# Optimization experiments

Hardware: AMD Instinct MI355X
Metric: run time of the kernel (lower is better)

## Reference

```python
import jax, jax.numpy as jnp
import numpy as np

N, E, D, R = 50000, 800000, 128, 16
NUM_OBJS, NUM_ATTRS, L = 179, 10, 5
OBJ_DIM, ATTR_DIM, HID, NANGLE = 96, 32, 512, 24


def setup_inputs() -> dict:
    key = jax.random.key(0)
    ks = jax.random.split(key, 20)
    z = jax.random.normal(ks[0], (N, D), dtype=jnp.float32)
    objs = jax.random.randint(ks[1], (N,), 0, NUM_OBJS + 1)
    s = jax.random.randint(ks[2], (E,), 0, N)
    o = jax.random.randint(ks[3], (E,), 0, N)
    p = jax.random.randint(ks[4], (E,), 0, R)
    triples = jnp.stack([s, p, o], axis=1)
    attributes = jax.random.randint(ks[5], (N,), 0, NUM_ATTRS)
    w = 0.05
    obj_emb = jax.random.normal(ks[6], (NUM_OBJS + 1, OBJ_DIM), dtype=jnp.float32)
    attr_emb = jax.random.normal(ks[7], (NUM_ATTRS, ATTR_DIM), dtype=jnp.float32)
    Wrel = jax.random.normal(ks[8], (L, R, D, D), dtype=jnp.float32) * w
    Wroot = jax.random.normal(ks[9], (L, D, D), dtype=jnp.float32) * w
    bconv = jnp.zeros((L, D), dtype=jnp.float32)
    box_W1 = jax.random.normal(ks[10], (2 * D + ATTR_DIM, HID), dtype=jnp.float32) * w
    box_b1 = jnp.zeros((HID,), dtype=jnp.float32)
    box_W2 = jax.random.normal(ks[11], (HID, 6), dtype=jnp.float32) * w
    box_b2 = jnp.zeros((6,), dtype=jnp.float32)
    ang_W1 = jax.random.normal(ks[12], (2 * D, HID), dtype=jnp.float32) * w
    ang_b1 = jnp.zeros((HID,), dtype=jnp.float32)
    ang_W2 = jax.random.normal(ks[13], (HID, NANGLE), dtype=jnp.float32) * w
    ang_b2 = jnp.zeros((NANGLE,), dtype=jnp.float32)
    return dict(z=z, objs=objs, triples=triples, attributes=attributes,
                obj_emb=obj_emb, attr_emb=attr_emb, Wrel=Wrel, Wroot=Wroot,
                bconv=bconv, box_W1=box_W1, box_b1=box_b1, box_W2=box_W2,
                box_b2=box_b2, ang_W1=ang_W1, ang_b1=ang_b1, ang_W2=ang_W2,
                ang_b2=ang_b2)


def _rgcn_layer(x, s, o, p, Wr, Wroot_l, b):
    # relation-typed transform of all nodes: [N, R, D]
    h_rel = jnp.einsum('nd,rdf->nrf', x, Wr)
    msgs = h_rel[s, p]                                   # [E, D] gather
    # mean aggregation per (target, relation), as in PyG RGCNConv
    seg = o * R + p
    cnt = jax.ops.segment_sum(jnp.ones((s.shape[0],), x.dtype), seg,
                              num_segments=x.shape[0] * R)
    deg = jnp.maximum(cnt[seg], 1.0)
    agg = jax.ops.segment_sum(msgs / deg[:, None], o, num_segments=x.shape[0])
    return x @ Wroot_l + agg + b


def reference(z, objs, triples, attributes, obj_emb, attr_emb, Wrel, Wroot,
              bconv, box_W1, box_b1, box_W2, box_b2, ang_W1, ang_b1,
              ang_W2, ang_b2):
    s, p, o = triples[:, 0], triples[:, 1], triples[:, 2]
    attr_vecs = attr_emb[attributes]                     # [N, 32]
    obj_vecs = jnp.concatenate([obj_emb[objs], attr_vecs], axis=1)  # [N, 128]
    for j in range(L):
        obj_vecs = jax.nn.relu(_rgcn_layer(obj_vecs, s, o, p,
                                           Wrel[j], Wroot[j], bconv[j]))
    obj_vecs = jnp.concatenate([obj_vecs, z], axis=1)    # [N, 256]
    obj_vecs_box = jnp.concatenate([obj_vecs, attr_vecs], axis=1)  # [N, 288]
    boxes_pred = jax.nn.relu(obj_vecs_box @ box_W1 + box_b1) @ box_W2 + box_b2
    ang_h = jax.nn.relu(obj_vecs @ ang_W1 + ang_b1) @ ang_W2 + ang_b2
    angles_pred = jax.nn.log_softmax(ang_h, axis=1)
    return boxes_pred, angles_pred
```

## Files before the change

kernel.cpp:

```cpp
#include <hip/hip_runtime.h>
#include <hip/hip_bf16.h>
#include <math.h>

#define NN   50000
#define EE   800000
#define RREL 16
#define LLAY 5
#define NBINS (NN * RREL)
#define HCAP 565248

typedef __attribute__((ext_vector_type(8))) short s8v;
typedef __attribute__((ext_vector_type(4))) float f4v;

__device__ __forceinline__ unsigned short f2bf(float f) {
  __hip_bfloat16 h = __float2bfloat16(f);
  return __builtin_bit_cast(unsigned short, h);
}
__device__ __forceinline__ float bf2f(unsigned int u) {
  return __builtin_bit_cast(float, u << 16);
}
__device__ __forceinline__ void split1(float v, unsigned short& h, unsigned short& l) {
  __hip_bfloat16 hb = __float2bfloat16(v);
  float hf = __bfloat162float(hb);
  h = __builtin_bit_cast(unsigned short, hb);
  __hip_bfloat16 lb = __float2bfloat16(v - hf);
  l = __builtin_bit_cast(unsigned short, lb);
}

__global__ void build_x0_kernel(const int* __restrict__ objs, const int* __restrict__ attrs,
                                const float* __restrict__ obj_emb, const float* __restrict__ attr_emb,
                                unsigned short* __restrict__ xh) {
  int t = blockIdx.x * blockDim.x + threadIdx.x;
  if (t >= NN * 32) return;
  int n = t >> 5, q = t & 31;
  float4 v;
  if (q < 24) v = *(const float4*)&obj_emb[(size_t)objs[n] * 96 + q * 4];
  else        v = *(const float4*)&attr_emb[(size_t)attrs[n] * 32 + (q - 24) * 4];
  ushort4 h;
  h.x = f2bf(v.x); h.y = f2bf(v.y); h.z = f2bf(v.z); h.w = f2bf(v.w);
  *(ushort4*)&xh[(size_t)n * 128 + q * 4] = h;
}

__global__ void prep_zattr(const float* __restrict__ z, const int* __restrict__ attrs,
                           const float* __restrict__ attr_emb,
                           unsigned short* __restrict__ zh, unsigned short* __restrict__ ah) {
  int t = blockIdx.x * blockDim.x + threadIdx.x;
  if (t >= NN * 40) return;
  int n = t / 40, q = t % 40;
  float4 v;
  ushort4 h;
  if (q < 32) {
    v = *(const float4*)&z[(size_t)n * 128 + q * 4];
    h.x = f2bf(v.x); h.y = f2bf(v.y); h.z = f2bf(v.z); h.w = f2bf(v.w);
    *(ushort4*)&zh[(size_t)n * 128 + q * 4] = h;
  } else {
    int qq = q - 32;
    v = *(const float4*)&attr_emb[(size_t)attrs[n] * 32 + qq * 4];
    h.x = f2bf(v.x); h.y = f2bf(v.y); h.z = f2bf(v.z); h.w = f2bf(v.w);
    *(ushort4*)&ah[(size_t)n * 32 + qq * 4] = h;
  }
}

__global__ void count_kernel(const int* __restrict__ triples, int* __restrict__ cnt) {
  int e = blockIdx.x * 256 + threadIdx.x;
  if (e >= EE) return;
  int p = triples[e * 3 + 1], o = triples[e * 3 + 2];
  atomicAdd(&cnt[o * RREL + p], 1);
}
__global__ void scanA(const int* __restrict__ cnt, int* __restrict__ binStart,
                      int* __restrict__ partial) {
  __shared__ int buf[1024];
  int g = blockIdx.x * 1024 + threadIdx.x;
  int v = (g < NBINS) ? cnt[g] : 0;
  buf[threadIdx.x] = v;
  __syncthreads();
  for (int d = 1; d < 1024; d <<= 1) {
    int t = (threadIdx.x >= d) ? buf[threadIdx.x - d] : 0;
    __syncthreads();
    buf[threadIdx.x] += t;
    __syncthreads();
  }
  if (g < NBINS) binStart[g] = buf[threadIdx.x] - v;
  if (threadIdx.x == 1023) partial[blockIdx.x] = buf[1023];
}
__global__ void scanB(int* __restrict__ partial, int* __restrict__ binStart, int nPart) {
  __shared__ int buf[1024];
  int v = (threadIdx.x < nPart) ? partial[threadIdx.x] : 0;
  buf[threadIdx.x] = v;
  __syncthreads();
  for (int d = 1; d < 1024; d <<= 1) {
    int t = (threadIdx.x >= d) ? buf[threadIdx.x - d] : 0;
    __syncthreads();
    buf[threadIdx.x] += t;
    __syncthreads();
  }
  if (threadIdx.x < nPart) partial[threadIdx.x] = buf[threadIdx.x] - v;
  if (threadIdx.x == 1023) binStart[NBINS] = buf[1023];
}
__global__ void scanC(int* __restrict__ binStart, const int* __restrict__ partial) {
  int g = blockIdx.x * 1024 + threadIdx.x;
  if (g < NBINS) binStart[g] += partial[blockIdx.x];
}

__global__ void mark_cells(const int* __restrict__ triples, int* __restrict__ sMark) {
  int e = blockIdx.x * 256 + threadIdx.x;
  if (e >= EE) return;
  int s = triples[e * 3 + 0], p = triples[e * 3 + 1];
  atomicAdd(&sMark[s * RREL + p], 1);
}
__global__ void count_dp(const int* __restrict__ sMark, int* __restrict__ Dp) {
  __shared__ int lh[RREL];
  if (threadIdx.x < RREL) lh[threadIdx.x] = 0;
  __syncthreads();
  int c = blockIdx.x * 256 + threadIdx.x;
  if (c < NBINS && sMark[c] > 0) atomicAdd(&lh[c & 15], 1);
  __syncthreads();
  if (threadIdx.x < RREL && lh[threadIdx.x] > 0)
    atomicAdd(&Dp[threadIdx.x], lh[threadIdx.x]);
}
__global__ void pad_scan(const int* __restrict__ Dp, int* __restrict__ pStart) {
  if (threadIdx.x == 0 && blockIdx.x == 0) {
    int s = 0;
    for (int p = 0; p < RREL; ++p) {
      pStart[p] = s;
      s += ((Dp[p] + 127) >> 7) << 7;
    }
    pStart[RREL] = s;
    s += ((NN + 127) >> 7) << 7;
    pStart[RREL + 1] = s;
  }
}
__global__ void assign_cells(int* __restrict__ sMark, const int* __restrict__ pStart,
                             int* __restrict__ pcur, int* __restrict__ spRel) {
  __shared__ int lh[RREL], lbase[RREL];
  if (threadIdx.x < RREL) lh[threadIdx.x] = 0;
  __syncthreads();
  int c = blockIdx.x * 256 + threadIdx.x;
  bool occ = (c < NBINS) && (sMark[c] > 0);
  int p = 0, my = 0;
  if (occ) { p = c & 15; my = atomicAdd(&lh[p], 1); }
  __syncthreads();
  if (threadIdx.x < RREL)
    lbase[threadIdx.x] = (lh[threadIdx.x] > 0)
                           ? atomicAdd(&pcur[threadIdx.x], lh[threadIdx.x]) : 0;
  __syncthreads();
  if (occ) {
    int cid = pStart[p] + lbase[p] + my;
    if (cid < HCAP) spRel[cid] = (c >> 4) * 32 + p;
    sMark[c] = cid + 1;
  }
}
__global__ void fill_root(const int* __restrict__ pStart, int* __restrict__ spRel) {
  int n = blockIdx.x * 256 + threadIdx.x;
  if (n >= NN) return;
  int cid = pStart[RREL] + n;
  if (cid < HCAP) spRel[cid] = n * 32 + 16;
}
__global__ void place_kernel(const int* __restrict__ triples, const int* __restrict__ cnt,
                             const int* __restrict__ binStart, int* __restrict__ cursor,
                             const int* __restrict__ sMark,
                             int* __restrict__ offD, float* __restrict__ wD) {
  int e = blockIdx.x * 256 + threadIdx.x;
  if (e >= EE) return;
  int s = triples[e * 3 + 0], p = triples[e * 3 + 1], o = triples[e * 3 + 2];
  int bin = o * RREL + p;
  int pos = binStart[bin] + atomicAdd(&cursor[bin], 1);
  int cid = sMark[s * RREL + p] - 1;
  offD[pos] = cid * 128;
  wD[pos] = 1.0f / (float)cnt[bin];
}

__global__ void prep_wrel(const float* __restrict__ Wrel, unsigned short* __restrict__ WT) {
  int t = blockIdx.x * 256 + threadIdx.x;
  if (t >= LLAY * RREL * 128 * 128) return;
  int f = t & 127, k = (t >> 7) & 127, lr = t >> 14;
  float v = Wrel[((size_t)lr * 128 + k) * 128 + f];
  WT[((size_t)lr * 128 + f) * 128 + k] = f2bf(v);
}
__global__ void prep_wroot(const float* __restrict__ Wroot, unsigned short* __restrict__ WT) {
  int t = blockIdx.x * 256 + threadIdx.x;
  if (t >= LLAY * 128 * 128) return;
  int f = t & 127, k = (t >> 7) & 127, l = t >> 14;
  float v = Wroot[((size_t)l * 128 + k) * 128 + f];
  WT[((size_t)l * 128 + f) * 128 + k] = f2bf(v);
}
__global__ void prep_wcat(const float* __restrict__ box_W1, const float* __restrict__ ang_W1,
                          unsigned short* __restrict__ WT) {
  int t = blockIdx.x * 256 + threadIdx.x;
  if (t >= 1024 * 288) return;
  int k = t % 288, c = t / 288;
  float v;
  if (c < 512) v = box_W1[(size_t)k * 512 + c];
  else         v = (k < 256) ? ang_W1[(size_t)k * 512 + (c - 512)] : 0.f;
  WT[(size_t)c * 288 + k] = f2bf(v);
}
__global__ void prep_bcat(const float* __restrict__ box_b1, const float* __restrict__ ang_b1,
                          float* __restrict__ bcat) {
  int t = blockIdx.x * 256 + threadIdx.x;
  if (t >= 1024) return;
  bcat[t] = (t < 512) ? box_b1[t] : ang_b1[t - 512];
}
__global__ void prep_w2cat(const float* __restrict__ box_W2, const float* __restrict__ ang_W2,
                           unsigned short* __restrict__ hi, unsigned short* __restrict__ lo) {
  int t = blockIdx.x * 256 + threadIdx.x;
  if (t >= 32 * 1024) return;
  int k = t & 1023, c = t >> 10;
  float v = 0.f;
  if (c < 6)       { if (k < 512)  v = box_W2[(size_t)k * 6 + c]; }
  else if (c < 30) { if (k >= 512) v = ang_W2[(size_t)(k - 512) * 24 + (c - 6)]; }
  split1(v, hi[(size_t)c * 1024 + k], lo[(size_t)c * 1024 + k]);
}

__global__ __launch_bounds__(256) void hrelc_mfma(const unsigned short* __restrict__ xh,
                                                  const int* __restrict__ spRel,
                                                  const unsigned short* __restrict__ Wt,
                                                  const unsigned short* __restrict__ Rt,
                                                  const float* __restrict__ bias,
                                                  const int* __restrict__ pStart,
                                                  unsigned short* __restrict__ Hc,
                                                  unsigned short* __restrict__ xr) {
  __shared__ __align__(16) unsigned short As[128][40];
  __shared__ __align__(16) unsigned short Bs[128][40];
  const int tid = threadIdx.x;
  const int row0 = blockIdx.x * 128;
  const int sr0 = spRel[row0];
  if (sr0 < 0) return;
  const int p = sr0 & 31;
  const bool isRoot = (p == 16);
  const unsigned short* WHp = isRoot ? Rt : Wt + (size_t)p * 128 * 128;

  const int wid = tid >> 6, lane = tid & 63;
  const int rg = wid >> 1, cg = wid & 1;
  const int lr = lane & 15, lk = (lane >> 4) * 8;
  f4v acc[4][4] = {};

  const int ar = tid >> 1, ahalf = tid & 1;
  const int aspv = spRel[row0 + ar];
  const int arow = (aspv >= 0) ? (aspv >> 5) : -1;
  s8v aR0, aR1;
  s8v bR[2];

  auto loadStep = [&](int k0) {
    if (arow >= 0) {
      aR0 = *(const s8v*)&xh[(size_t)arow * 128 + k0 + ahalf * 16];
      aR1 = *(const s8v*)&xh[(size_t)arow * 128 + k0 + ahalf * 16 + 8];
    } else {
      s8v zz = {0,0,0,0,0,0,0,0}; aR0 = zz; aR1 = zz;
    }
#pragma unroll
    for (int i = 0; i < 2; ++i) {
      int idx = tid + i * 256;
      int c = idx >> 2, c8 = (idx & 3) * 8;
      bR[i] = *(const s8v*)&WHp[(size_t)c * 128 + k0 + c8];
    }
  };
  auto writeStep = [&]() {
    *(s8v*)&As[ar][ahalf * 16]     = aR0;
    *(s8v*)&As[ar][ahalf * 16 + 8] = aR1;
#pragma unroll
    for (int i = 0; i < 2; ++i) {
      int idx = tid + i * 256;
      int c = idx >> 2, c8 = (idx & 3) * 8;
      *(s8v*)&Bs[c][c8] = bR[i];
    }
  };

  loadStep(0);
  for (int k0 = 0; k0 < 128; k0 += 32) {
    __syncthreads();
    writeStep();
    __syncthreads();
    if (k0 < 96) loadStep(k0 + 32);

    s8v ah[4];
#pragma unroll
    for (int mf = 0; mf < 4; ++mf) ah[mf] = *(s8v*)&As[rg * 64 + mf * 16 + lr][lk];
#pragma unroll
    for (int nf = 0; nf < 4; ++nf) {
      s8v bh_ = *(s8v*)&Bs[cg * 64 + nf * 16 + lr][lk];
#pragma unroll
      for (int mf = 0; mf < 4; ++mf) {
        acc[mf][nf] = __builtin_amdgcn_mfma_f32_16x16x32_bf16(ah[mf], bh_, acc[mf][nf], 0, 0, 0);
      }
    }
  }

  if (!isRoot) {
#pragma unroll
    for (int mf = 0; mf < 4; ++mf)
#pragma unroll
      for (int nf = 0; nf < 4; ++nf) {
        f4v v = acc[mf][nf];
        int rbase = row0 + rg * 64 + mf * 16 + (lane >> 4) * 4;
        int col = cg * 64 + nf * 16 + lr;
#pragma unroll
        for (int q = 0; q < 4; ++q)
          Hc[(size_t)(rbase + q) * 128 + col] = f2bf(v[q]);
      }
  } else {
    const int rootBase = pStart[RREL];
#pragma unroll
    for (int mf = 0; mf < 4; ++mf)
#pragma unroll
      for (int nf = 0; nf < 4; ++nf) {
        f4v v = acc[mf][nf];
        int rbase = row0 + rg * 64 + mf * 16 + (lane >> 4) * 4;
        int col = cg * 64 + nf * 16 + lr;
        float b = bias[col];
#pragma unroll
        for (int q = 0; q < 4; ++q) {
          int node = rbase + q - rootBase;
          if (node >= 0 && node < NN)
            xr[(size_t)node * 128 + col] = f2bf(v[q] + b);
        }
      }
  }
}

__global__ __launch_bounds__(256) void mlpcat_mfma(const unsigned short* __restrict__ xh,
                                                   const unsigned short* __restrict__ zh,
                                                   const unsigned short* __restrict__ ath,
                                                   const unsigned short* __restrict__ Wt,
                                                   const float* __restrict__ bcat,
                                                   const unsigned short* __restrict__ W2H,
                                                   const unsigned short* __restrict__ W2L,
                                                   float* __restrict__ logitsPart) {
  __shared__ __align__(16) char smem[25600];
  auto As = (unsigned short(*)[40])smem;
  auto Bs = (unsigned short(*)[40])(smem + 5120);
  auto ht = (unsigned short(*)[80])smem;
  auto red = (float(*)[33])(smem + 10240);
  const int tid = threadIdx.x;
  const int row0 = blockIdx.y * 64;
  const int cb = blockIdx.x;
  const int wid = tid >> 6, lane = tid & 63;
  const int wcol = wid * 64;
  const int lr = lane & 15, lk = (lane >> 4) * 8;
  f4v acc[4][4] = {};

  s8v aR;
  s8v bR[4];
  const int ar = tid >> 2, ac8 = (tid & 3) * 8;
  const int an = row0 + ar;

  auto loadStep = [&](int k0) {
    if (an < NN) {
      if (k0 < 128)      aR = *(const s8v*)&xh[(size_t)an * 128 + k0 + ac8];
      else if (k0 < 256) aR = *(const s8v*)&zh[(size_t)an * 128 + (k0 - 128) + ac8];
      else               aR = *(const s8v*)&ath[(size_t)an * 32 + (k0 - 256) + ac8];
    } else { s8v zz = {0, 0, 0, 0, 0, 0, 0, 0}; aR = zz; }
#pragma unroll
    for (int i = 0; i < 4; ++i) {
      int idx = tid + i * 256;
      int c = idx >> 2, c8 = (idx & 3) * 8;
      int gc = cb * 256 + c;
      bR[i] = *(const s8v*)&Wt[(size_t)gc * 288 + k0 + c8];
    }
  };
  auto writeStep = [&]() {
    *(s8v*)&As[ar][ac8] = aR;
#pragma unroll
    for (int i = 0; i < 4; ++i) {
      int idx = tid + i * 256;
      int c = idx >> 2, c8 = (idx & 3) * 8;
      *(s8v*)&Bs[c][c8] = bR[i];
    }
  };

  loadStep(0);
  for (int step = 0; step < 9; ++step) {
    __syncthreads();
    writeStep();
    __syncthreads();
    if (step < 8) loadStep((step + 1) * 32);

    s8v ah[4];
#pragma unroll
    for (int mf = 0; mf < 4; ++mf) ah[mf] = *(s8v*)&As[mf * 16 + lr][lk];
#pragma unroll
    for (int nf = 0; nf < 4; ++nf) {
      s8v bh_ = *(s8v*)&Bs[wcol + nf * 16 + lr][lk];
#pragma unroll
      for (int mf = 0; mf < 4; ++mf) {
        acc[mf][nf] = __builtin_amdgcn_mfma_f32_16x16x32_bf16(ah[mf], bh_, acc[mf][nf], 0, 0, 0);
      }
    }
  }

#pragma unroll
  for (int mf = 0; mf < 4; ++mf)
#pragma unroll
    for (int nf = 0; nf < 4; ++nf) {
      int gc = cb * 256 + wcol + nf * 16 + lr;
      float b = bcat[gc];
#pragma unroll
      for (int q = 0; q < 4; ++q)
        acc[mf][nf][q] = fmaxf(acc[mf][nf][q] + b, 0.f);
    }

  for (int w = 0; w < 4; ++w) {
    __syncthreads();
    if (wid == w) {
#pragma unroll
      for (int mf = 0; mf < 4; ++mf)
#pragma unroll
        for (int nf = 0; nf < 4; ++nf)
#pragma unroll
          for (int q = 0; q < 4; ++q)
            ht[mf * 16 + (lane >> 4) * 4 + q][nf * 16 + lr] = f2bf(acc[mf][nf][q]);

      f4v acc2[4][2] = {};
#pragma unroll
      for (int ks = 0; ks < 2; ++ks) {
        s8v a_[4];
#pragma unroll
        for (int mfp = 0; mfp < 4; ++mfp)
          a_[mfp] = *(s8v*)&ht[mfp * 16 + lr][ks * 32 + lk];
#pragma unroll
        for (int nfp = 0; nfp < 2; ++nfp) {
          int kg = cb * 256 + wcol + ks * 32 + lk;
          int n = nfp * 16 + lr;
          s8v bh_ = *(const s8v*)&W2H[(size_t)n * 1024 + kg];
          s8v bl_ = *(const s8v*)&W2L[(size_t)n * 1024 + kg];
#pragma unroll
          for (int mfp = 0; mfp < 4; ++mfp) {
            acc2[mfp][nfp] = __builtin_amdgcn_mfma_f32_16x16x32_bf16(a_[mfp], bh_, acc2[mfp][nfp], 0, 0, 0);
            acc2[mfp][nfp] = __builtin_amdgcn_mfma_f32_16x16x32_bf16(a_[mfp], bl_, acc2[mfp][nfp], 0, 0, 0);
          }
        }
      }
#pragma unroll
      for (int mfp = 0; mfp < 4; ++mfp)
#pragma unroll
        for (int nfp = 0; nfp < 2; ++nfp)
#pragma unroll
          for (int q = 0; q < 4; ++q) {
            int node = mfp * 16 + (lane >> 4) * 4 + q;
            int L = nfp * 16 + lr;
            if (w == 0) red[node][L] = acc2[mfp][nfp][q];
            else        red[node][L] += acc2[mfp][nfp][q];
          }
    }
  }
  __syncthreads();
#pragma unroll
  for (int i = 0; i < 8; ++i) {
    int t = tid * 8 + i;
    int node = t >> 5, L = t & 31;
    int rr = row0 + node;
    if (rr < NN) logitsPart[((size_t)cb * NN + rr) * 32 + L] = red[node][L];
  }
}

__global__ void head_post(const float* __restrict__ logitsPart, const float* __restrict__ box_b2,
                          const float* __restrict__ ang_b2, float* __restrict__ out) {
  int n = blockIdx.x * 256 + threadIdx.x;
  if (n >= NN) return;
  float l[32];
#pragma unroll
  for (int i = 0; i < 8; ++i)
    *(float4*)&l[i * 4] = *(const float4*)&logitsPart[(size_t)n * 32 + i * 4];
#pragma unroll
  for (int cb = 1; cb < 4; ++cb) {
#pragma unroll
    for (int i = 0; i < 8; ++i) {
      float4 v = *(const float4*)&logitsPart[((size_t)cb * NN + n) * 32 + i * 4];
      l[i * 4 + 0] += v.x; l[i * 4 + 1] += v.y;
      l[i * 4 + 2] += v.z; l[i * 4 + 3] += v.w;
    }
  }
  float* ob = out + (size_t)n * 6;
#pragma unroll
  for (int c = 0; c < 6; ++c) ob[c] = l[c] + box_b2[c];
  float a[24];
  float mx = -1e30f;
#pragma unroll
  for (int c = 0; c < 24; ++c) { a[c] = l[6 + c] + ang_b2[c]; mx = fmaxf(mx, a[c]); }
  float ssum = 0.f;
#pragma unroll
  for (int c = 0; c < 24; ++c) ssum += expf(a[c] - mx);
  float lse = mx + logf(ssum);
  float* oa = out + (size_t)NN * 6 + (size_t)n * 24;
#pragma unroll
  for (int c = 0; c < 24; ++c) oa[c] = a[c] - lse;
}

__global__ __launch_bounds__(256) void gather_kernel(const unsigned short* __restrict__ Hc,
                                                     const int* __restrict__ binStart,
                                                     const int* __restrict__ offD,
                                                     const float* __restrict__ wD,
                                                     const unsigned short* __restrict__ xr,
                                                     unsigned short* __restrict__ xh) {
  int wid = threadIdx.x >> 6, lane = threadIdx.x & 63;
  int o = blockIdx.x * 4 + wid;
  if (o >= NN) return;
  int beg = binStart[o * RREL];
  int end = binStart[o * RREL + RREL];
  float a0 = 0.f, a1 = 0.f, b0 = 0.f, b1 = 0.f;
  float c0 = 0.f, c1 = 0.f, d0 = 0.f, d1 = 0.f;
  int i = beg;
  for (; i + 3 < end; i += 4) {
    int of1 = offD[i], of2 = offD[i + 1], of3 = offD[i + 2], of4 = offD[i + 3];
    float w1 = wD[i], w2 = wD[i + 1], w3 = wD[i + 2], w4 = wD[i + 3];
    unsigned int u1 = *(const unsigned int*)&Hc[of1 + lane * 2];
    unsigned int u2 = *(const unsigned int*)&Hc[of2 + lane * 2];
    unsigned int u3 = *(const unsigned int*)&Hc[of3 + lane * 2];
    unsigned int u4 = *(const unsigned int*)&Hc[of4 + lane * 2];
    a0 += w1 * bf2f(u1 & 0xffffu);
    a1 += w1 * bf2f(u1 >> 16);
    b0 += w2 * bf2f(u2 & 0xffffu);
    b1 += w2 * bf2f(u2 >> 16);
    c0 += w3 * bf2f(u3 & 0xffffu);
    c1 += w3 * bf2f(u3 >> 16);
    d0 += w4 * bf2f(u4 & 0xffffu);
    d1 += w4 * bf2f(u4 >> 16);
  }
  for (; i < end; ++i) {
    int of1 = offD[i];
    float w1 = wD[i];
    unsigned int u1 = *(const unsigned int*)&Hc[of1 + lane * 2];
    a0 += w1 * bf2f(u1 & 0xffffu);
    a1 += w1 * bf2f(u1 >> 16);
  }
  a0 += b0 + c0 + d0;
  a1 += b1 + c1 + d1;
  unsigned int ur = *(const unsigned int*)&xr[(size_t)o * 128 + lane * 2];
  float r0 = bf2f(ur & 0xffffu) + a0;
  float r1 = bf2f(ur >> 16) + a1;
  r0 = fmaxf(r0, 0.f); r1 = fmaxf(r1, 0.f);
  unsigned int pk = (unsigned int)f2bf(r0) | ((unsigned int)f2bf(r1) << 16);
  *(unsigned int*)&xh[(size_t)o * 128 + lane * 2] = pk;
}

extern "C" void kernel_launch(void* const* d_in, const int* in_sizes, int n_in,
                              void* d_out, int out_size, void* d_ws, size_t ws_size,
                              hipStream_t stream) {
  const float* z        = (const float*)d_in[0];
  const int*   objs     = (const int*)d_in[1];
  const int*   triples  = (const int*)d_in[2];
  const int*   attrs    = (const int*)d_in[3];
  const float* obj_emb  = (const float*)d_in[4];
  const float* attr_emb = (const float*)d_in[5];
  const float* Wrel     = (const float*)d_in[6];
  const float* Wroot    = (const float*)d_in[7];
  const float* bconv    = (const float*)d_in[8];
  const float* box_W1   = (const float*)d_in[9];
  const float* box_b1   = (const float*)d_in[10];
  const float* box_W2   = (const float*)d_in[11];
  const float* box_b2   = (const float*)d_in[12];
  const float* ang_W1   = (const float*)d_in[13];
  const float* ang_b1   = (const float*)d_in[14];
  const float* ang_W2   = (const float*)d_in[15];
  const float* ang_b2   = (const float*)d_in[16];
  float* out = (float*)d_out;

  char* base = (char*)d_ws;
  size_t cur = 0;
  auto alloc = [&](size_t bytes) -> char* {
    char* p = base + cur;
    cur += (bytes + 255) & ~(size_t)255;
    return p;
  };
  unsigned short* Hc   = (unsigned short*)alloc((size_t)HCAP * 128 * 2);
  unsigned short* xr   = (unsigned short*)alloc((size_t)NN * 128 * 2);
  unsigned short* xhi  = (unsigned short*)alloc((size_t)NN * 128 * 2);
  unsigned short* zhi  = (unsigned short*)alloc((size_t)NN * 128 * 2);
  unsigned short* athi = (unsigned short*)alloc((size_t)NN * 32 * 2);
  unsigned short* WThi = (unsigned short*)alloc((size_t)LLAY * RREL * 128 * 128 * 2);
  unsigned short* WrtH = (unsigned short*)alloc((size_t)LLAY * 128 * 128 * 2);
  unsigned short* WcH  = (unsigned short*)alloc((size_t)1024 * 288 * 2);
  unsigned short* W2H  = (unsigned short*)alloc((size_t)32 * 1024 * 2);
  unsigned short* W2L  = (unsigned short*)alloc((size_t)32 * 1024 * 2);
  float* bcat          = (float*)alloc(1024 * 4);
  float* logitsPart    = (float*)alloc((size_t)4 * NN * 32 * 4);
  int*   cnt      = (int*)alloc((size_t)NBINS * 4);
  int*   binStart = (int*)alloc((size_t)(NBINS + 1) * 4);
  int*   cursor   = (int*)alloc((size_t)NBINS * 4);
  int*   sMark    = (int*)alloc((size_t)NBINS * 4);
  int*   spRel    = (int*)alloc((size_t)HCAP * 4);
  int*   partial  = (int*)alloc(4096);
  int*   meta     = (int*)alloc(256);
  int*   offD     = (int*)alloc((size_t)EE * 4);
  float* wD       = (float*)alloc((size_t)EE * 4);
  int* Dp = meta, *pStart = meta + 16, *pcur = meta + 40;

  hipMemsetAsync(cnt, 0, (size_t)NBINS * 4, stream);
  hipMemsetAsync(cursor, 0, (size_t)NBINS * 4, stream);
  hipMemsetAsync(sMark, 0, (size_t)NBINS * 4, stream);
  hipMemsetAsync(meta, 0, 256, stream);
  hipMemsetAsync(spRel, 0xFF, (size_t)HCAP * 4, stream);

  build_x0_kernel<<<(NN * 32 + 255) / 256, 256, 0, stream>>>(objs, attrs, obj_emb, attr_emb, xhi);
  prep_zattr<<<(NN * 40 + 255) / 256, 256, 0, stream>>>(z, attrs, attr_emb, zhi, athi);
  count_kernel<<<(EE + 255) / 256, 256, 0, stream>>>(triples, cnt);
  const int nPart = (NBINS + 1023) / 1024;
  scanA<<<nPart, 1024, 0, stream>>>(cnt, binStart, partial);
  scanB<<<1, 1024, 0, stream>>>(partial, binStart, nPart);
  scanC<<<nPart, 1024, 0, stream>>>(binStart, partial);
  mark_cells<<<(EE + 255) / 256, 256, 0, stream>>>(triples, sMark);
  count_dp<<<(NBINS + 255) / 256, 256, 0, stream>>>(sMark, Dp);
  pad_scan<<<1, 64, 0, stream>>>(Dp, pStart);
  assign_cells<<<(NBINS + 255) / 256, 256, 0, stream>>>(sMark, pStart, pcur, spRel);
  fill_root<<<(NN + 255) / 256, 256, 0, stream>>>(pStart, spRel);
  place_kernel<<<(EE + 255) / 256, 256, 0, stream>>>(triples, cnt, binStart, cursor, sMark,
                                                     offD, wD);
  prep_wrel<<<(LLAY * RREL * 128 * 128 + 255) / 256, 256, 0, stream>>>(Wrel, WThi);
  prep_wroot<<<(LLAY * 128 * 128 + 255) / 256, 256, 0, stream>>>(Wroot, WrtH);
  prep_wcat<<<(1024 * 288 + 255) / 256, 256, 0, stream>>>(box_W1, ang_W1, WcH);
  prep_bcat<<<4, 256, 0, stream>>>(box_b1, ang_b1, bcat);
  prep_w2cat<<<(32 * 1024 + 255) / 256, 256, 0, stream>>>(box_W2, ang_W2, W2H, W2L);

  const int rowBlocks = (NN + 63) / 64;
  for (int j = 0; j < LLAY; ++j) {
    hrelc_mfma<<<HCAP / 128, 256, 0, stream>>>(xhi, spRel,
                                               WThi + (size_t)j * RREL * 128 * 128,
                                               WrtH + (size_t)j * 128 * 128,
                                               bconv + (size_t)j * 128, pStart, Hc, xr);
    gather_kernel<<<(NN + 3) / 4, 256, 0, stream>>>(Hc, binStart, offD, wD, xr, xhi);
  }

  mlpcat_mfma<<<dim3(4, rowBlocks), 256, 0, stream>>>(xhi, zhi, athi, WcH, bcat,
                                                      W2H, W2L, logitsPart);
  head_post<<<(NN + 255) / 256, 256, 0, stream>>>(logitsPart, box_b2, ang_b2, out);
}
```

Baseline: 852.3 us.

## Fuse count/mark kernels, widen hrelc K-tile, parallelize head second-stage reduction

Merges the two edge atomic-count kernels into one pass over triples, saving a launch and a second read of the triples array. The relation GEMM now stages K in chunks of 64 instead of 32, halving the number of sync/load rounds at the cost of more shared memory and registers. The head kernel's second GEMM no longer serializes its four waves through one shared tile; each wave uses a private tile and the partial results are combined with shared-memory float atomics. That adds atomic contention and makes the floating-point summation order nondeterministic.

```diff
diff --git a/kernel.cpp b/kernel.cpp
--- a/kernel.cpp
+++ b/kernel.cpp
@@ -61,11 +61,13 @@
   }
 }
 
-__global__ void count_kernel(const int* __restrict__ triples, int* __restrict__ cnt) {
+__global__ void count_mark(const int* __restrict__ triples, int* __restrict__ cnt,
+                           int* __restrict__ sMark) {
   int e = blockIdx.x * 256 + threadIdx.x;
   if (e >= EE) return;
-  int p = triples[e * 3 + 1], o = triples[e * 3 + 2];
+  int s = triples[e * 3 + 0], p = triples[e * 3 + 1], o = triples[e * 3 + 2];
   atomicAdd(&cnt[o * RREL + p], 1);
+  atomicAdd(&sMark[s * RREL + p], 1);
 }
 __global__ void scanA(const int* __restrict__ cnt, int* __restrict__ binStart,
                       int* __restrict__ partial) {
@@ -102,12 +104,6 @@
   if (g < NBINS) binStart[g] += partial[blockIdx.x];
 }
 
-__global__ void mark_cells(const int* __restrict__ triples, int* __restrict__ sMark) {
-  int e = blockIdx.x * 256 + threadIdx.x;
-  if (e >= EE) return;
-  int s = triples[e * 3 + 0], p = triples[e * 3 + 1];
-  atomicAdd(&sMark[s * RREL + p], 1);
-}
 __global__ void count_dp(const int* __restrict__ sMark, int* __restrict__ Dp) {
   __shared__ int lh[RREL];
   if (threadIdx.x < RREL) lh[threadIdx.x] = 0;
@@ -219,8 +215,8 @@
                                                   const int* __restrict__ pStart,
                                                   unsigned short* __restrict__ Hc,
                                                   unsigned short* __restrict__ xr) {
-  __shared__ __align__(16) unsigned short As[128][40];
-  __shared__ __align__(16) unsigned short Bs[128][40];
+  __shared__ __align__(16) unsigned short As[128][72];
+  __shared__ __align__(16) unsigned short Bs[128][72];
   const int tid = threadIdx.x;
   const int row0 = blockIdx.x * 128;
   const int sr0 = spRel[row0];
@@ -234,53 +230,49 @@
   const int lr = lane & 15, lk = (lane >> 4) * 8;
   f4v acc[4][4] = {};
 
-  const int ar = tid >> 1, ahalf = tid & 1;
-  const int aspv = spRel[row0 + ar];
-  const int arow = (aspv >= 0) ? (aspv >> 5) : -1;
-  s8v aR0, aR1;
-  s8v bR[2];
+  const int sr = tid >> 3, sc8 = (tid & 7) * 8;
+  int arow[4];
+#pragma unroll
+  for (int i = 0; i < 4; ++i) {
+    int v = spRel[row0 + sr + 32 * i];
+    arow[i] = (v >= 0) ? (v >> 5) : -1;
+  }
+  s8v aR[4], bR[4];
 
   auto loadStep = [&](int k0) {
-    if (arow >= 0) {
-      aR0 = *(const s8v*)&xh[(size_t)arow * 128 + k0 + ahalf * 16];
-      aR1 = *(const s8v*)&xh[(size_t)arow * 128 + k0 + ahalf * 16 + 8];
-    } else {
-      s8v zz = {0,0,0,0,0,0,0,0}; aR0 = zz; aR1 = zz;
-    }
-#pragma unroll
-    for (int i = 0; i < 2; ++i) {
-      int idx = tid + i * 256;
-      int c = idx >> 2, c8 = (idx & 3) * 8;
-      bR[i] = *(const s8v*)&WHp[(size_t)c * 128 + k0 + c8];
+#pragma unroll
+    for (int i = 0; i < 4; ++i) {
+      if (arow[i] >= 0) aR[i] = *(const s8v*)&xh[(size_t)arow[i] * 128 + k0 + sc8];
+      else { s8v zz = {0,0,0,0,0,0,0,0}; aR[i] = zz; }
+      bR[i] = *(const s8v*)&WHp[(size_t)(sr + 32 * i) * 128 + k0 + sc8];
     }
   };
   auto writeStep = [&]() {
-    *(s8v*)&As[ar][ahalf * 16]     = aR0;
-    *(s8v*)&As[ar][ahalf * 16 + 8] = aR1;
-#pragma unroll
-    for (int i = 0; i < 2; ++i) {
-      int idx = tid + i * 256;
-      int c = idx >> 2, c8 = (idx & 3) * 8;
-      *(s8v*)&Bs[c][c8] = bR[i];
+#pragma unroll
+    for (int i = 0; i < 4; ++i) {
+      *(s8v*)&As[sr + 32 * i][sc8] = aR[i];
+      *(s8v*)&Bs[sr + 32 * i][sc8] = bR[i];
     }
   };
 
   loadStep(0);
-  for (int k0 = 0; k0 < 128; k0 += 32) {
+  for (int k0 = 0; k0 < 128; k0 += 64) {
     __syncthreads();
     writeStep();
     __syncthreads();
-    if (k0 < 96) loadStep(k0 + 32);
-
-    s8v ah[4];
-#pragma unroll
-    for (int mf = 0; mf < 4; ++mf) ah[mf] = *(s8v*)&As[rg * 64 + mf * 16 + lr][lk];
-#pragma unroll
-    for (int nf = 0; nf < 4; ++nf) {
-      s8v bh_ = *(s8v*)&Bs[cg * 64 + nf * 16 + lr][lk];
-#pragma unroll
-      for (int mf = 0; mf < 4; ++mf) {
-        acc[mf][nf] = __builtin_amdgcn_mfma_f32_16x16x32_bf16(ah[mf], bh_, acc[mf][nf], 0, 0, 0);
+    if (k0 == 0) loadStep(64);
+#pragma unroll
+    for (int ks = 0; ks < 2; ++ks) {
+      s8v ah[4];
+#pragma unroll
+      for (int mf = 0; mf < 4; ++mf)
+        ah[mf] = *(s8v*)&As[rg * 64 + mf * 16 + lr][ks * 32 + lk];
+#pragma unroll
+      for (int nf = 0; nf < 4; ++nf) {
+        s8v bh_ = *(s8v*)&Bs[cg * 64 + nf * 16 + lr][ks * 32 + lk];
+#pragma unroll
+        for (int mf = 0; mf < 4; ++mf)
+          acc[mf][nf] = __builtin_amdgcn_mfma_f32_16x16x32_bf16(ah[mf], bh_, acc[mf][nf], 0, 0, 0);
       }
     }
   }
@@ -328,8 +320,6 @@
   __shared__ __align__(16) char smem[25600];
   auto As = (unsigned short(*)[40])smem;
   auto Bs = (unsigned short(*)[40])(smem + 5120);
-  auto ht = (unsigned short(*)[80])smem;
-  auto red = (float(*)[33])(smem + 10240);
   const int tid = threadIdx.x;
   const int row0 = blockIdx.y * 64;
   const int cb = blockIdx.x;
@@ -398,50 +388,54 @@
         acc[mf][nf][q] = fmaxf(acc[mf][nf][q] + b, 0.f);
     }
 
-  for (int w = 0; w < 4; ++w) {
-    __syncthreads();
-    if (wid == w) {
-#pragma unroll
-      for (int mf = 0; mf < 4; ++mf)
-#pragma unroll
-        for (int nf = 0; nf < 4; ++nf)
-#pragma unroll
-          for (int q = 0; q < 4; ++q)
-            ht[mf * 16 + (lane >> 4) * 4 + q][nf * 16 + lr] = f2bf(acc[mf][nf][q]);
-
-      f4v acc2[4][2] = {};
-#pragma unroll
-      for (int ks = 0; ks < 2; ++ks) {
-        s8v a_[4];
-#pragma unroll
-        for (int mfp = 0; mfp < 4; ++mfp)
-          a_[mfp] = *(s8v*)&ht[mfp * 16 + lr][ks * 32 + lk];
-#pragma unroll
-        for (int nfp = 0; nfp < 2; ++nfp) {
-          int kg = cb * 256 + wcol + ks * 32 + lk;
-          int n = nfp * 16 + lr;
-          s8v bh_ = *(const s8v*)&W2H[(size_t)n * 1024 + kg];
-          s8v bl_ = *(const s8v*)&W2L[(size_t)n * 1024 + kg];
-#pragma unroll
-          for (int mfp = 0; mfp < 4; ++mfp) {
-            acc2[mfp][nfp] = __builtin_amdgcn_mfma_f32_16x16x32_bf16(a_[mfp], bh_, acc2[mfp][nfp], 0, 0, 0);
-            acc2[mfp][nfp] = __builtin_amdgcn_mfma_f32_16x16x32_bf16(a_[mfp], bl_, acc2[mfp][nfp], 0, 0, 0);
-          }
-        }
+  auto ht  = (unsigned short(*)[34])(smem + wid * 4352);
+  auto red = (float(*)[32])(smem + 17408);
+  __syncthreads();
+  {
+    float* rp = (float*)(smem + 17408);
+#pragma unroll
+    for (int i = 0; i < 8; ++i) rp[tid + i * 256] = 0.f;
+  }
+  __syncthreads();
+
+  f4v acc2[4][2] = {};
+#pragma unroll
+  for (int ks = 0; ks < 2; ++ks) {
+#pragma unroll
+    for (int mf = 0; mf < 4; ++mf)
+#pragma unroll
+      for (int nfh = 0; nfh < 2; ++nfh) {
+        int nf = ks * 2 + nfh;
+#pragma unroll
+        for (int q = 0; q < 4; ++q)
+          ht[mf * 16 + (lane >> 4) * 4 + q][nfh * 16 + lr] = f2bf(acc[mf][nf][q]);
       }
-#pragma unroll
-      for (int mfp = 0; mfp < 4; ++mfp)
-#pragma unroll
-        for (int nfp = 0; nfp < 2; ++nfp)
-#pragma unroll
-          for (int q = 0; q < 4; ++q) {
-            int node = mfp * 16 + (lane >> 4) * 4 + q;
-            int L = nfp * 16 + lr;
-            if (w == 0) red[node][L] = acc2[mfp][nfp][q];
-            else        red[node][L] += acc2[mfp][nfp][q];
-          }
-    }
-  }
+    s8v a_[4];
+#pragma unroll
+    for (int mfp = 0; mfp < 4; ++mfp) a_[mfp] = *(s8v*)&ht[mfp * 16 + lr][lk];
+    int kg = cb * 256 + wcol + ks * 32 + lk;
+#pragma unroll
+    for (int nfp = 0; nfp < 2; ++nfp) {
+      int n = nfp * 16 + lr;
+      s8v bh_ = *(const s8v*)&W2H[(size_t)n * 1024 + kg];
+      s8v bl_ = *(const s8v*)&W2L[(size_t)n * 1024 + kg];
+#pragma unroll
+      for (int mfp = 0; mfp < 4; ++mfp) {
+        acc2[mfp][nfp] = __builtin_amdgcn_mfma_f32_16x16x32_bf16(a_[mfp], bh_, acc2[mfp][nfp], 0, 0, 0);
+        acc2[mfp][nfp] = __builtin_amdgcn_mfma_f32_16x16x32_bf16(a_[mfp], bl_, acc2[mfp][nfp], 0, 0, 0);
+      }
+    }
+  }
+#pragma unroll
+  for (int mfp = 0; mfp < 4; ++mfp)
+#pragma unroll
+    for (int nfp = 0; nfp < 2; ++nfp)
+#pragma unroll
+      for (int q = 0; q < 4; ++q) {
+        int node = mfp * 16 + (lane >> 4) * 4 + q;
+        int L = nfp * 16 + lr;
+        atomicAdd(&red[node][L], acc2[mfp][nfp][q]);
+      }
   __syncthreads();
 #pragma unroll
   for (int i = 0; i < 8; ++i) {
@@ -592,12 +586,11 @@
 
   build_x0_kernel<<<(NN * 32 + 255) / 256, 256, 0, stream>>>(objs, attrs, obj_emb, attr_emb, xhi);
   prep_zattr<<<(NN * 40 + 255) / 256, 256, 0, stream>>>(z, attrs, attr_emb, zhi, athi);
-  count_kernel<<<(EE + 255) / 256, 256, 0, stream>>>(triples, cnt);
+  count_mark<<<(EE + 255) / 256, 256, 0, stream>>>(triples, cnt, sMark);
   const int nPart = (NBINS + 1023) / 1024;
   scanA<<<nPart, 1024, 0, stream>>>(cnt, binStart, partial);
   scanB<<<1, 1024, 0, stream>>>(partial, binStart, nPart);
   scanC<<<nPart, 1024, 0, stream>>>(binStart, partial);
-  mark_cells<<<(EE + 255) / 256, 256, 0, stream>>>(triples, sMark);
   count_dp<<<(NBINS + 255) / 256, 256, 0, stream>>>(sMark, Dp);
   pad_scan<<<1, 64, 0, stream>>>(Dp, pStart);
   assign_cells<<<(NBINS + 255) / 256, 256, 0, stream>>>(sMark, pStart, pcur, spRel);
```

Measured after the change: 952.5 us. +11.8%, slower.
